# Kernel tuning notes

Hardware: AMD Instinct MI355X
Metric: run time of the kernel (lower is better)

## Reference

```python
import jax, jax.numpy as jnp
import numpy as np

N, E, HID, INP = 100000, 1600000, 64, 3
BN_EPS = 1e-5


def _bn(h, gamma, beta):
    # BatchNorm1d in training mode: biased batch stats over dim 0
    m = jnp.mean(h, axis=0)
    v = jnp.mean((h - m) ** 2, axis=0)
    return (h - m) * jax.lax.rsqrt(v + BN_EPS) * gamma + beta


def setup_inputs() -> dict:
    key = jax.random.key(0)
    ks = jax.random.split(key, 16)
    d_in = INP + HID  # 67
    s1 = 1.0 / np.sqrt(d_in)
    s2 = 1.0 / np.sqrt(HID)
    return {
        "x": jax.random.normal(ks[0], (N, INP), jnp.float32),
        "edge_index": jax.random.randint(ks[1], (2, E), 0, N, jnp.int64),
        "edge_attr": jax.random.normal(ks[2], (E, HID), jnp.float32),
        "u": jax.random.normal(ks[3], (1, 16), jnp.float32),
        "batch": jnp.zeros((N,), jnp.int64),
        # node_mlp_1: Linear(67,64), BN(64), ReLU, Linear(64,64)
        "w1": jax.random.uniform(ks[4], (d_in, HID), jnp.float32, -s1, s1),
        "b1": jax.random.uniform(ks[5], (HID,), jnp.float32, -s1, s1),
        "g1": jnp.ones((HID,), jnp.float32),
        "be1": jnp.zeros((HID,), jnp.float32),
        "w2": jax.random.uniform(ks[6], (HID, HID), jnp.float32, -s2, s2),
        "b2": jax.random.uniform(ks[7], (HID,), jnp.float32, -s2, s2),
        # node_mlp_2: Linear(67,64), BN(64), ReLU, Linear(64,64)
        "w3": jax.random.uniform(ks[8], (d_in, HID), jnp.float32, -s1, s1),
        "b3": jax.random.uniform(ks[9], (HID,), jnp.float32, -s1, s1),
        "g3": jnp.ones((HID,), jnp.float32),
        "be3": jnp.zeros((HID,), jnp.float32),
        "w4": jax.random.uniform(ks[10], (HID, HID), jnp.float32, -s2, s2),
        "b4": jax.random.uniform(ks[11], (HID,), jnp.float32, -s2, s2),
    }


def reference(x, edge_index, edge_attr, u, batch,
              w1, b1, g1, be1, w2, b2,
              w3, b3, g3, be3, w4, b4):
    row, col = edge_index[0], edge_index[1]
    n = x.shape[0]
    # gather source nodes, concat with edge features -> edge MLP
    h = jnp.concatenate([x[row], edge_attr], axis=1)          # [E, 67]
    h = _bn(h @ w1 + b1, g1, be1)
    h = jax.nn.relu(h) @ w2 + b2                              # [E, 64]
    # scatter_mean by destination node (0 for isolated nodes)
    s = jax.ops.segment_sum(h, col, num_segments=n)           # [N, 64]
    cnt = jax.ops.segment_sum(jnp.ones((h.shape[0],), h.dtype), col, num_segments=n)
    agg = s / jnp.maximum(cnt, 1.0)[:, None]
    # node MLP
    o = jnp.concatenate([x, agg], axis=1)                     # [N, 67]
    o = _bn(o @ w3 + b3, g3, be3)
    return jax.nn.relu(o) @ w4 + b4                           # [N, 64]
```

## Files before the change

### kernel.cpp

```cpp
#include <hip/hip_runtime.h>


#define HID 64
#define KPAD 104
#define RPAD 72
#define BN_EPS 1e-5f

typedef __attribute__((ext_vector_type(8))) short bf16x8;
typedef __attribute__((ext_vector_type(4))) short bf16x4;
typedef __attribute__((ext_vector_type(4))) float f32x4;

static __device__ __forceinline__ short f2bf(float f) {
  union { float fv; unsigned u; } v; v.fv = f;
  unsigned r = v.u + 0x7FFFu + ((v.u >> 16) & 1u);
  return (short)(r >> 16);
}

static __device__ __forceinline__ void stage_w_k96(short (*W)[KPAD], const float* __restrict__ w, int tid) {
  for (int i = tid; i < 64 * KPAD; i += 256) {
    int n = i / KPAD, k = i - n * KPAD;
    float v = 0.f;
    if (k < 64)      v = w[(size_t)(3 + k) * HID + n];
    else if (k < 67) v = w[(size_t)(k - 64) * HID + n];
    W[n][k] = f2bf(v);
  }
}

static __device__ __forceinline__ void stage_w_k64(short (*W)[RPAD], const float* __restrict__ w, int tid) {
  for (int i = tid; i < 64 * RPAD; i += 256) {
    int n = i / RPAD, k = i - n * RPAD;
    float v = (k < 64) ? w[(size_t)k * HID + n] : 0.f;
    W[n][k] = f2bf(v);
  }
}

static __device__ __forceinline__ void gemm_k96(const short (*A)[KPAD], const short (*W)[KPAD],
                                                int wv, int l15, int kg, f32x4* acc) {
  const int ar = wv * 16 + l15;
  #pragma unroll
  for (int ks = 0; ks < 3; ++ks) {
    bf16x8 a = *(const bf16x8*)&A[ar][ks * 32 + kg * 8];
    #pragma unroll
    for (int j = 0; j < 4; ++j) {
      bf16x8 b = *(const bf16x8*)&W[j * 16 + l15][ks * 32 + kg * 8];
      acc[j] = __builtin_amdgcn_mfma_f32_16x16x32_bf16(a, b, acc[j], 0, 0, 0);
    }
  }
}

static __device__ __forceinline__ void gemm_k64(const short (*A)[RPAD], const short (*W)[RPAD],
                                                int wv, int l15, int kg, f32x4* acc) {
  const int ar = wv * 16 + l15;
  #pragma unroll
  for (int ks = 0; ks < 2; ++ks) {
    bf16x8 a = *(const bf16x8*)&A[ar][ks * 32 + kg * 8];
    #pragma unroll
    for (int j = 0; j < 4; ++j) {
      bf16x8 b = *(const bf16x8*)&W[j * 16 + l15][ks * 32 + kg * 8];
      acc[j] = __builtin_amdgcn_mfma_f32_16x16x32_bf16(a, b, acc[j], 0, 0, 0);
    }
  }
}

static __device__ __forceinline__ void stage_edge_A(short (*A)[KPAD], const float* __restrict__ attr,
                                                    const int* __restrict__ ei_row,
                                                    const float* __restrict__ x,
                                                    long e0, int E, int tid) {
  #pragma unroll
  for (int u = 0; u < 4; ++u) {
    int f4 = tid + u * 256;
    int r = f4 >> 4, c4 = (f4 & 15) << 2;
    long e = e0 + r;
    float4 v = make_float4(0.f, 0.f, 0.f, 0.f);
    if (e < E) v = *reinterpret_cast<const float4*>(attr + (size_t)e * HID + c4);
    bf16x4 s; s[0] = f2bf(v.x); s[1] = f2bf(v.y); s[2] = f2bf(v.z); s[3] = f2bf(v.w);
    *reinterpret_cast<bf16x4*>(&A[r][c4]) = s;
  }
  if (tid < 64) {
    long e = e0 + tid;
    float x0 = 0.f, x1 = 0.f, x2 = 0.f;
    if (e < E) {
      int nd = ei_row[e];
      x0 = x[nd * 3]; x1 = x[nd * 3 + 1]; x2 = x[nd * 3 + 2];
    }
    A[tid][64] = f2bf(x0); A[tid][65] = f2bf(x1); A[tid][66] = f2bf(x2);
  }
}

static __device__ __forceinline__ void stage_node_A(short (*A)[KPAD], const float* __restrict__ aggsum,
                                                    const float* __restrict__ cnt,
                                                    const float* __restrict__ x,
                                                    long n0, int N, int tid) {
  #pragma unroll
  for (int u = 0; u < 4; ++u) {
    int f4 = tid + u * 256;
    int r = f4 >> 4, c4 = (f4 & 15) << 2;
    long n = n0 + r;
    float4 v = make_float4(0.f, 0.f, 0.f, 0.f);
    if (n < N) {
      float ic = 1.f / fmaxf(cnt[n], 1.f);
      const float4 t = *reinterpret_cast<const float4*>(aggsum + (size_t)n * HID + c4);
      v.x = t.x * ic; v.y = t.y * ic; v.z = t.z * ic; v.w = t.w * ic;
    }
    bf16x4 s; s[0] = f2bf(v.x); s[1] = f2bf(v.y); s[2] = f2bf(v.z); s[3] = f2bf(v.w);
    *reinterpret_cast<bf16x4*>(&A[r][c4]) = s;
  }
  if (tid < 64) {
    long n = n0 + tid;
    float x0 = 0.f, x1 = 0.f, x2 = 0.f;
    if (n < N) { x0 = x[n * 3]; x1 = x[n * 3 + 1]; x2 = x[n * 3 + 2]; }
    A[tid][64] = f2bf(x0); A[tid][65] = f2bf(x1); A[tid][66] = f2bf(x2);
  }
}

__global__ __launch_bounds__(256) void k_edge_stats(
    const float* __restrict__ attr, const int* __restrict__ ei_row,
    const float* __restrict__ x, const float* __restrict__ w1,
    float* __restrict__ gsum, float* __restrict__ gsq, int E, int numTiles) {
  __shared__ short A[64][KPAD];
  __shared__ short W1s[64][KPAD];
  __shared__ float redS[64], redQ[64];

  const int tid = threadIdx.x;
  const int lane = tid & 63, wv = tid >> 6;
  const int l15 = lane & 15, kg = lane >> 4;

  for (int i = tid; i < 64 * KPAD; i += 256) ((short*)A)[i] = 0;
  stage_w_k96(W1s, w1, tid);
  if (tid < 64) { redS[tid] = 0.f; redQ[tid] = 0.f; }

  float rs[4] = {0.f, 0.f, 0.f, 0.f};
  float rq[4] = {0.f, 0.f, 0.f, 0.f};

  for (int tile = blockIdx.x; tile < numTiles; tile += gridDim.x) {
    __syncthreads();
    stage_edge_A(A, attr, ei_row, x, (long)tile * 64, E, tid);
    __syncthreads();
    f32x4 acc[4];
    const f32x4 z = {0.f, 0.f, 0.f, 0.f};
    acc[0] = z; acc[1] = z; acc[2] = z; acc[3] = z;
    gemm_k96(A, W1s, wv, l15, kg, acc);
    #pragma unroll
    for (int j = 0; j < 4; ++j) {
      float s = 0.f, q = 0.f;
      #pragma unroll
      for (int rg = 0; rg < 4; ++rg) { float v = acc[j][rg]; s += v; q += v * v; }
      rs[j] += s; rq[j] += q;
    }
  }
  __syncthreads();
  #pragma unroll
  for (int j = 0; j < 4; ++j) {
    atomicAdd(&redS[j * 16 + l15], rs[j]);
    atomicAdd(&redQ[j * 16 + l15], rq[j]);
  }
  __syncthreads();
  if (tid < 64) { atomicAdd(&gsum[tid], redS[tid]); atomicAdd(&gsq[tid], redQ[tid]); }
}

__global__ void k_finalize(const float* __restrict__ gsum, const float* __restrict__ gsq,
                           const float* __restrict__ g, const float* __restrict__ be,
                           float* __restrict__ scale, float* __restrict__ shift, float denom) {
  int t = threadIdx.x;
  if (t < 64) {
    float m = gsum[t] / denom;
    float var = gsq[t] / denom - m * m;
    float is = rsqrtf(var + BN_EPS);
    float sc = g[t] * is;
    scale[t] = sc;
    shift[t] = be[t] - m * sc;
  }
}

__global__ __launch_bounds__(256) void k_edge_main(
    const float* __restrict__ attr, const int* __restrict__ ei_row,
    const int* __restrict__ ei_col, const float* __restrict__ x,
    const float* __restrict__ w1, const float* __restrict__ w2,
    const float* __restrict__ b2, const float* __restrict__ scaleE,
    const float* __restrict__ shiftE,
    float* __restrict__ aggsum, float* __restrict__ cnt, int E, int numTiles) {
  __shared__ short A[64][KPAD];
  __shared__ short W1s[64][KPAD];
  __shared__ short R[64][RPAD];
  __shared__ short W2s[64][RPAD];
  __shared__ float sclS[64], shtS[64], b2S[64];
  __shared__ int colS[64];

  const int tid = threadIdx.x;
  const int lane = tid & 63, wv = tid >> 6;
  const int l15 = lane & 15, kg = lane >> 4;

  for (int i = tid; i < 64 * KPAD; i += 256) ((short*)A)[i] = 0;
  stage_w_k96(W1s, w1, tid);
  stage_w_k64(W2s, w2, tid);
  if (tid < 64) { sclS[tid] = scaleE[tid]; shtS[tid] = shiftE[tid]; b2S[tid] = b2[tid]; }

  const f32x4 z = {0.f, 0.f, 0.f, 0.f};

  for (int tile = blockIdx.x; tile < numTiles; tile += gridDim.x) {
    __syncthreads();
    stage_edge_A(A, attr, ei_row, x, (long)tile * 64, E, tid);
    if (tid < 64) {
      long e = (long)tile * 64 + tid;
      int c = (e < E) ? ei_col[e] : -1;
      colS[tid] = c;
      if (c >= 0) atomicAdd(&cnt[c], 1.f);
    }
    __syncthreads();

    f32x4 acc1[4];
    acc1[0] = z; acc1[1] = z; acc1[2] = z; acc1[3] = z;
    gemm_k96(A, W1s, wv, l15, kg, acc1);

    #pragma unroll
    for (int j = 0; j < 4; ++j) {
      int c = j * 16 + l15;
      float sc = sclS[c], sh = shtS[c];
      #pragma unroll
      for (int rg = 0; rg < 4; ++rg) {
        float v = fmaxf(acc1[j][rg] * sc + sh, 0.f);
        R[wv * 16 + kg * 4 + rg][c] = f2bf(v);
      }
    }
    __syncthreads();

    f32x4 acc2[4];
    acc2[0] = z; acc2[1] = z; acc2[2] = z; acc2[3] = z;
    gemm_k64(R, W2s, wv, l15, kg, acc2);

    #pragma unroll
    for (int j = 0; j < 4; ++j) {
      int c = j * 16 + l15;
      float bb = b2S[c];
      #pragma unroll
      for (int rg = 0; rg < 4; ++rg) {
        int nd = colS[wv * 16 + kg * 4 + rg];
        if (nd >= 0) atomicAdd(&aggsum[(size_t)nd * HID + c], acc2[j][rg] + bb);
      }
    }
  }
}

__global__ __launch_bounds__(256) void k_node_stats(
    const float* __restrict__ aggsum, const float* __restrict__ cnt,
    const float* __restrict__ x, const float* __restrict__ w3,
    float* __restrict__ gsum, float* __restrict__ gsq, int N, int numTiles) {
  __shared__ short A[64][KPAD];
  __shared__ short W3s[64][KPAD];
  __shared__ float redS[64], redQ[64];

  const int tid = threadIdx.x;
  const int lane = tid & 63, wv = tid >> 6;
  const int l15 = lane & 15, kg = lane >> 4;

  for (int i = tid; i < 64 * KPAD; i += 256) ((short*)A)[i] = 0;
  stage_w_k96(W3s, w3, tid);
  if (tid < 64) { redS[tid] = 0.f; redQ[tid] = 0.f; }

  float rs[4] = {0.f, 0.f, 0.f, 0.f};
  float rq[4] = {0.f, 0.f, 0.f, 0.f};

  for (int tile = blockIdx.x; tile < numTiles; tile += gridDim.x) {
    __syncthreads();
    stage_node_A(A, aggsum, cnt, x, (long)tile * 64, N, tid);
    __syncthreads();
    f32x4 acc[4];
    const f32x4 z = {0.f, 0.f, 0.f, 0.f};
    acc[0] = z; acc[1] = z; acc[2] = z; acc[3] = z;
    gemm_k96(A, W3s, wv, l15, kg, acc);
    #pragma unroll
    for (int j = 0; j < 4; ++j) {
      float s = 0.f, q = 0.f;
      #pragma unroll
      for (int rg = 0; rg < 4; ++rg) { float v = acc[j][rg]; s += v; q += v * v; }
      rs[j] += s; rq[j] += q;
    }
  }
  __syncthreads();
  #pragma unroll
  for (int j = 0; j < 4; ++j) {
    atomicAdd(&redS[j * 16 + l15], rs[j]);
    atomicAdd(&redQ[j * 16 + l15], rq[j]);
  }
  __syncthreads();
  if (tid < 64) { atomicAdd(&gsum[tid], redS[tid]); atomicAdd(&gsq[tid], redQ[tid]); }
}

__global__ __launch_bounds__(256) void k_node_main(
    const float* __restrict__ aggsum, const float* __restrict__ cnt,
    const float* __restrict__ x, const float* __restrict__ w3,
    const float* __restrict__ w4, const float* __restrict__ b4,
    const float* __restrict__ scaleN, const float* __restrict__ shiftN,
    float* __restrict__ out, int N, int numTiles) {
  __shared__ short A[64][KPAD];
  __shared__ short W3s[64][KPAD];
  __shared__ short R[64][RPAD];
  __shared__ short W4s[64][RPAD];
  __shared__ float sclS[64], shtS[64], b4S[64];

  const int tid = threadIdx.x;
  const int lane = tid & 63, wv = tid >> 6;
  const int l15 = lane & 15, kg = lane >> 4;

  for (int i = tid; i < 64 * KPAD; i += 256) ((short*)A)[i] = 0;
  stage_w_k96(W3s, w3, tid);
  stage_w_k64(W4s, w4, tid);
  if (tid < 64) { sclS[tid] = scaleN[tid]; shtS[tid] = shiftN[tid]; b4S[tid] = b4[tid]; }

  const f32x4 z = {0.f, 0.f, 0.f, 0.f};

  for (int tile = blockIdx.x; tile < numTiles; tile += gridDim.x) {
    __syncthreads();
    stage_node_A(A, aggsum, cnt, x, (long)tile * 64, N, tid);
    __syncthreads();

    f32x4 acc1[4];
    acc1[0] = z; acc1[1] = z; acc1[2] = z; acc1[3] = z;
    gemm_k96(A, W3s, wv, l15, kg, acc1);

    #pragma unroll
    for (int j = 0; j < 4; ++j) {
      int c = j * 16 + l15;
      float sc = sclS[c], sh = shtS[c];
      #pragma unroll
      for (int rg = 0; rg < 4; ++rg) {
        float v = fmaxf(acc1[j][rg] * sc + sh, 0.f);
        R[wv * 16 + kg * 4 + rg][c] = f2bf(v);
      }
    }
    __syncthreads();

    f32x4 acc2[4];
    acc2[0] = z; acc2[1] = z; acc2[2] = z; acc2[3] = z;
    gemm_k64(R, W4s, wv, l15, kg, acc2);

    long n0 = (long)tile * 64;
    #pragma unroll
    for (int j = 0; j < 4; ++j) {
      int c = j * 16 + l15;
      float bb = b4S[c];
      #pragma unroll
      for (int rg = 0; rg < 4; ++rg) {
        long n = n0 + wv * 16 + kg * 4 + rg;
        if (n < N) out[(size_t)n * HID + c] = acc2[j][rg] + bb;
      }
    }
  }
}

extern "C" void kernel_launch(void* const* d_in, const int* in_sizes, int n_in,
                              void* d_out, int out_size, void* d_ws, size_t ws_size,
                              hipStream_t stream) {
  const float* x    = (const float*)d_in[0];
  const int*   ei   = (const int*)d_in[1];
  const float* attr = (const float*)d_in[2];
  const float* w1   = (const float*)d_in[5];
  const float* g1   = (const float*)d_in[7];
  const float* be1  = (const float*)d_in[8];
  const float* w2   = (const float*)d_in[9];
  const float* b2   = (const float*)d_in[10];
  const float* w3   = (const float*)d_in[11];
  const float* g3   = (const float*)d_in[13];
  const float* be3  = (const float*)d_in[14];
  const float* w4   = (const float*)d_in[15];
  const float* b4   = (const float*)d_in[16];
  float* out = (float*)d_out;

  const int N = in_sizes[0] / 3;
  const int E = in_sizes[1] / 2;

  float* wsf = (float*)d_ws;
  float* gsumE  = wsf + 0;
  float* gsqE   = wsf + 64;
  float* scaleE = wsf + 128;
  float* shiftE = wsf + 192;
  float* gsumN  = wsf + 256;
  float* gsqN   = wsf + 320;
  float* scaleN = wsf + 384;
  float* shiftN = wsf + 448;
  float* aggsum = wsf + 512;
  float* cnt    = wsf + 512 + (size_t)N * HID;

  hipMemsetAsync(d_ws, 0, (512 + (size_t)N * HID + (size_t)N) * sizeof(float), stream);

  const int tilesE = (E + 63) / 64;
  const int tilesN = (N + 63) / 64;
  const int gridE = tilesE < 2048 ? tilesE : 2048;

  k_edge_stats<<<gridE, 256, 0, stream>>>(attr, ei, x, w1, gsumE, gsqE, E, tilesE);
  k_finalize<<<1, 64, 0, stream>>>(gsumE, gsqE, g1, be1, scaleE, shiftE, (float)E);
  k_edge_main<<<gridE, 256, 0, stream>>>(attr, ei, ei + E, x, w1, w2, b2, scaleE, shiftE,
                                         aggsum, cnt, E, tilesE);
  k_node_stats<<<tilesN, 256, 0, stream>>>(aggsum, cnt, x, w3, gsumN, gsqN, N, tilesN);
  k_finalize<<<1, 64, 0, stream>>>(gsumN, gsqN, g3, be3, scaleN, shiftN, (float)N);
  k_node_main<<<tilesN, 256, 0, stream>>>(aggsum, cnt, x, w3, w4, b4, scaleN, shiftN, out, N, tilesN);
}
```

Baseline: 1.211 ms.

## Scatter ReLU activations before second linear, fp16 atomics, register-resident weights

Uses the linearity of the second edge Linear to scatter-add the post-ReLU activations per destination node and apply W2 and b2 once per node in a new kernel. This removes the per-edge second GEMM and cuts atomic traffic. Scatter atomics now use packed half2 in an fp16 accumulator, halving scatter bytes. Weights are held as MFMA B fragments in registers with wave-level 16-row tiles instead of shared-memory staging and block barriers, and node activations are stored as bf16. The fp16 accumulation risks precision loss and overflow on high-degree nodes.

```diff
diff --git a/kernel.cpp b/kernel.cpp
--- a/kernel.cpp
+++ b/kernel.cpp
@@ -1,8 +1,8 @@
 #include <hip/hip_runtime.h>
+#include <hip/hip_fp16.h>
 
 
 #define HID 64
-#define KPAD 104
 #define RPAD 72
 #define BN_EPS 1e-5f
 
@@ -16,130 +16,113 @@
   return (short)(r >> 16);
 }
 
-static __device__ __forceinline__ void stage_w_k96(short (*W)[KPAD], const float* __restrict__ w, int tid) {
-  for (int i = tid; i < 64 * KPAD; i += 256) {
-    int n = i / KPAD, k = i - n * KPAD;
-    float v = 0.f;
-    if (k < 64)      v = w[(size_t)(3 + k) * HID + n];
-    else if (k < 67) v = w[(size_t)(k - 64) * HID + n];
-    W[n][k] = f2bf(v);
-  }
-}
-
-static __device__ __forceinline__ void stage_w_k64(short (*W)[RPAD], const float* __restrict__ w, int tid) {
-  for (int i = tid; i < 64 * RPAD; i += 256) {
-    int n = i / RPAD, k = i - n * RPAD;
-    float v = (k < 64) ? w[(size_t)k * HID + n] : 0.f;
-    W[n][k] = f2bf(v);
-  }
-}
-
-static __device__ __forceinline__ void gemm_k96(const short (*A)[KPAD], const short (*W)[KPAD],
-                                                int wv, int l15, int kg, f32x4* acc) {
-  const int ar = wv * 16 + l15;
+#define Z8 {0,0,0,0,0,0,0,0}
+
+static __device__ __forceinline__ void load_B96(bf16x8 Bf[3][4], const float* __restrict__ w,
+                                                int l15, int kg) {
   #pragma unroll
-  for (int ks = 0; ks < 3; ++ks) {
-    bf16x8 a = *(const bf16x8*)&A[ar][ks * 32 + kg * 8];
-    #pragma unroll
-    for (int j = 0; j < 4; ++j) {
-      bf16x8 b = *(const bf16x8*)&W[j * 16 + l15][ks * 32 + kg * 8];
-      acc[j] = __builtin_amdgcn_mfma_f32_16x16x32_bf16(a, b, acc[j], 0, 0, 0);
-    }
-  }
-}
-
-static __device__ __forceinline__ void gemm_k64(const short (*A)[RPAD], const short (*W)[RPAD],
-                                                int wv, int l15, int kg, f32x4* acc) {
-  const int ar = wv * 16 + l15;
+  for (int ks = 0; ks < 3; ++ks)
+    #pragma unroll
+    for (int j = 0; j < 4; ++j) {
+      bf16x8 b = Z8;
+      #pragma unroll
+      for (int jj = 0; jj < 8; ++jj) {
+        int k = ks * 32 + kg * 8 + jj;
+        int n = 4 * l15 + j;
+        float v = 0.f;
+        if (k < 64)      v = w[(size_t)(3 + k) * HID + n];
+        else if (k < 67) v = w[(size_t)(k - 64) * HID + n];
+        b[jj] = f2bf(v);
+      }
+      Bf[ks][j] = b;
+    }
+}
+
+static __device__ __forceinline__ void load_B64(bf16x8 Bf[2][4], const float* __restrict__ w,
+                                                int l15, int kg) {
   #pragma unroll
-  for (int ks = 0; ks < 2; ++ks) {
-    bf16x8 a = *(const bf16x8*)&A[ar][ks * 32 + kg * 8];
-    #pragma unroll
-    for (int j = 0; j < 4; ++j) {
-      bf16x8 b = *(const bf16x8*)&W[j * 16 + l15][ks * 32 + kg * 8];
-      acc[j] = __builtin_amdgcn_mfma_f32_16x16x32_bf16(a, b, acc[j], 0, 0, 0);
-    }
-  }
-}
-
-static __device__ __forceinline__ void stage_edge_A(short (*A)[KPAD], const float* __restrict__ attr,
-                                                    const int* __restrict__ ei_row,
-                                                    const float* __restrict__ x,
-                                                    long e0, int E, int tid) {
-  #pragma unroll
-  for (int u = 0; u < 4; ++u) {
-    int f4 = tid + u * 256;
-    int r = f4 >> 4, c4 = (f4 & 15) << 2;
-    long e = e0 + r;
-    float4 v = make_float4(0.f, 0.f, 0.f, 0.f);
-    if (e < E) v = *reinterpret_cast<const float4*>(attr + (size_t)e * HID + c4);
-    bf16x4 s; s[0] = f2bf(v.x); s[1] = f2bf(v.y); s[2] = f2bf(v.z); s[3] = f2bf(v.w);
-    *reinterpret_cast<bf16x4*>(&A[r][c4]) = s;
-  }
-  if (tid < 64) {
-    long e = e0 + tid;
-    float x0 = 0.f, x1 = 0.f, x2 = 0.f;
-    if (e < E) {
+  for (int ks = 0; ks < 2; ++ks)
+    #pragma unroll
+    for (int j = 0; j < 4; ++j) {
+      bf16x8 b = Z8;
+      #pragma unroll
+      for (int jj = 0; jj < 8; ++jj) {
+        int k = ks * 32 + kg * 8 + jj;
+        int n = 4 * l15 + j;
+        b[jj] = f2bf(w[(size_t)k * HID + n]);
+      }
+      Bf[ks][j] = b;
+    }
+}
+
+static __device__ __forceinline__ void edge_A(bf16x8 A[3], const float* __restrict__ attr,
+                                              const int* __restrict__ ei_row,
+                                              const float* __restrict__ x,
+                                              long e0, int E, int l15, int kg) {
+  bf16x8 a0 = Z8, a1 = Z8, a2 = Z8;
+  long e = e0 + l15;
+  if (e < E) {
+    const float* ar = attr + (size_t)e * HID + kg * 8;
+    f32x4 p0 = *(const f32x4*)(ar);
+    f32x4 p1 = *(const f32x4*)(ar + 4);
+    f32x4 p2 = *(const f32x4*)(ar + 32);
+    f32x4 p3 = *(const f32x4*)(ar + 36);
+    #pragma unroll
+    for (int t = 0; t < 4; ++t) {
+      a0[t] = f2bf(p0[t]); a0[4 + t] = f2bf(p1[t]);
+      a1[t] = f2bf(p2[t]); a1[4 + t] = f2bf(p3[t]);
+    }
+    if (kg == 0) {
       int nd = ei_row[e];
-      x0 = x[nd * 3]; x1 = x[nd * 3 + 1]; x2 = x[nd * 3 + 2];
-    }
-    A[tid][64] = f2bf(x0); A[tid][65] = f2bf(x1); A[tid][66] = f2bf(x2);
-  }
-}
-
-static __device__ __forceinline__ void stage_node_A(short (*A)[KPAD], const float* __restrict__ aggsum,
-                                                    const float* __restrict__ cnt,
-                                                    const float* __restrict__ x,
-                                                    long n0, int N, int tid) {
-  #pragma unroll
-  for (int u = 0; u < 4; ++u) {
-    int f4 = tid + u * 256;
-    int r = f4 >> 4, c4 = (f4 & 15) << 2;
-    long n = n0 + r;
-    float4 v = make_float4(0.f, 0.f, 0.f, 0.f);
-    if (n < N) {
-      float ic = 1.f / fmaxf(cnt[n], 1.f);
-      const float4 t = *reinterpret_cast<const float4*>(aggsum + (size_t)n * HID + c4);
-      v.x = t.x * ic; v.y = t.y * ic; v.z = t.z * ic; v.w = t.w * ic;
-    }
-    bf16x4 s; s[0] = f2bf(v.x); s[1] = f2bf(v.y); s[2] = f2bf(v.z); s[3] = f2bf(v.w);
-    *reinterpret_cast<bf16x4*>(&A[r][c4]) = s;
-  }
-  if (tid < 64) {
-    long n = n0 + tid;
-    float x0 = 0.f, x1 = 0.f, x2 = 0.f;
-    if (n < N) { x0 = x[n * 3]; x1 = x[n * 3 + 1]; x2 = x[n * 3 + 2]; }
-    A[tid][64] = f2bf(x0); A[tid][65] = f2bf(x1); A[tid][66] = f2bf(x2);
-  }
+      a2[0] = f2bf(x[(size_t)nd * 3]);
+      a2[1] = f2bf(x[(size_t)nd * 3 + 1]);
+      a2[2] = f2bf(x[(size_t)nd * 3 + 2]);
+    }
+  }
+  A[0] = a0; A[1] = a1; A[2] = a2;
+}
+
+static __device__ __forceinline__ void node_A(bf16x8 A[3], const short* __restrict__ aggb,
+                                              const float* __restrict__ x,
+                                              long n0, int N, int l15, int kg) {
+  bf16x8 a0 = Z8, a1 = Z8, a2 = Z8;
+  long n = n0 + l15;
+  if (n < N) {
+    a0 = *(const bf16x8*)(aggb + (size_t)n * HID + kg * 8);
+    a1 = *(const bf16x8*)(aggb + (size_t)n * HID + 32 + kg * 8);
+    if (kg == 0) {
+      a2[0] = f2bf(x[(size_t)n * 3]);
+      a2[1] = f2bf(x[(size_t)n * 3 + 1]);
+      a2[2] = f2bf(x[(size_t)n * 3 + 2]);
+    }
+  }
+  A[0] = a0; A[1] = a1; A[2] = a2;
 }
 
 __global__ __launch_bounds__(256) void k_edge_stats(
     const float* __restrict__ attr, const int* __restrict__ ei_row,
     const float* __restrict__ x, const float* __restrict__ w1,
     float* __restrict__ gsum, float* __restrict__ gsq, int E, int numTiles) {
-  __shared__ short A[64][KPAD];
-  __shared__ short W1s[64][KPAD];
-  __shared__ float redS[64], redQ[64];
-
   const int tid = threadIdx.x;
-  const int lane = tid & 63, wv = tid >> 6;
+  const int wv = tid >> 6, lane = tid & 63;
   const int l15 = lane & 15, kg = lane >> 4;
-
-  for (int i = tid; i < 64 * KPAD; i += 256) ((short*)A)[i] = 0;
-  stage_w_k96(W1s, w1, tid);
-  if (tid < 64) { redS[tid] = 0.f; redQ[tid] = 0.f; }
+  bf16x8 B[3][4];
+  load_B96(B, w1, l15, kg);
 
   float rs[4] = {0.f, 0.f, 0.f, 0.f};
   float rq[4] = {0.f, 0.f, 0.f, 0.f};
-
-  for (int tile = blockIdx.x; tile < numTiles; tile += gridDim.x) {
-    __syncthreads();
-    stage_edge_A(A, attr, ei_row, x, (long)tile * 64, E, tid);
-    __syncthreads();
-    f32x4 acc[4];
-    const f32x4 z = {0.f, 0.f, 0.f, 0.f};
-    acc[0] = z; acc[1] = z; acc[2] = z; acc[3] = z;
-    gemm_k96(A, W1s, wv, l15, kg, acc);
+  const f32x4 z = {0.f, 0.f, 0.f, 0.f};
+  const int wstride = gridDim.x * 4;
+
+  for (int t = blockIdx.x * 4 + wv; t < numTiles; t += wstride) {
+    bf16x8 A[3];
+    edge_A(A, attr, ei_row, x, (long)t * 16, E, l15, kg);
+    f32x4 acc[4]; acc[0] = z; acc[1] = z; acc[2] = z; acc[3] = z;
+    #pragma unroll
+    for (int ks = 0; ks < 3; ++ks)
+      #pragma unroll
+      for (int j = 0; j < 4; ++j)
+        acc[j] = __builtin_amdgcn_mfma_f32_16x16x32_bf16(A[ks], B[ks][j], acc[j], 0, 0, 0);
     #pragma unroll
     for (int j = 0; j < 4; ++j) {
       float s = 0.f, q = 0.f;
@@ -148,14 +131,18 @@
       rs[j] += s; rq[j] += q;
     }
   }
-  __syncthreads();
   #pragma unroll
   for (int j = 0; j < 4; ++j) {
-    atomicAdd(&redS[j * 16 + l15], rs[j]);
-    atomicAdd(&redQ[j * 16 + l15], rq[j]);
-  }
-  __syncthreads();
-  if (tid < 64) { atomicAdd(&gsum[tid], redS[tid]); atomicAdd(&gsq[tid], redQ[tid]); }
+    rs[j] += __shfl_xor(rs[j], 16); rs[j] += __shfl_xor(rs[j], 32);
+    rq[j] += __shfl_xor(rq[j], 16); rq[j] += __shfl_xor(rq[j], 32);
+  }
+  if (lane < 16) {
+    #pragma unroll
+    for (int j = 0; j < 4; ++j) {
+      atomicAdd(&gsum[4 * lane + j], rs[j]);
+      atomicAdd(&gsq[4 * lane + j], rq[j]);
+    }
+  }
 }
 
 __global__ void k_finalize(const float* __restrict__ gsum, const float* __restrict__ gsq,
@@ -175,99 +162,144 @@
 __global__ __launch_bounds__(256) void k_edge_main(
     const float* __restrict__ attr, const int* __restrict__ ei_row,
     const int* __restrict__ ei_col, const float* __restrict__ x,
-    const float* __restrict__ w1, const float* __restrict__ w2,
-    const float* __restrict__ b2, const float* __restrict__ scaleE,
+    const float* __restrict__ w1, const float* __restrict__ scaleE,
     const float* __restrict__ shiftE,
-    float* __restrict__ aggsum, float* __restrict__ cnt, int E, int numTiles) {
-  __shared__ short A[64][KPAD];
-  __shared__ short W1s[64][KPAD];
-  __shared__ short R[64][RPAD];
-  __shared__ short W2s[64][RPAD];
-  __shared__ float sclS[64], shtS[64], b2S[64];
-  __shared__ int colS[64];
-
+    __half* __restrict__ rsum, float* __restrict__ cnt, int E, int numTiles) {
   const int tid = threadIdx.x;
-  const int lane = tid & 63, wv = tid >> 6;
+  const int wv = tid >> 6, lane = tid & 63;
   const int l15 = lane & 15, kg = lane >> 4;
-
-  for (int i = tid; i < 64 * KPAD; i += 256) ((short*)A)[i] = 0;
-  stage_w_k96(W1s, w1, tid);
-  stage_w_k64(W2s, w2, tid);
-  if (tid < 64) { sclS[tid] = scaleE[tid]; shtS[tid] = shiftE[tid]; b2S[tid] = b2[tid]; }
+  bf16x8 B[3][4];
+  load_B96(B, w1, l15, kg);
+  const f32x4 scv = *(const f32x4*)(scaleE + 4 * l15);
+  const f32x4 shv = *(const f32x4*)(shiftE + 4 * l15);
 
   const f32x4 z = {0.f, 0.f, 0.f, 0.f};
-
-  for (int tile = blockIdx.x; tile < numTiles; tile += gridDim.x) {
-    __syncthreads();
-    stage_edge_A(A, attr, ei_row, x, (long)tile * 64, E, tid);
-    if (tid < 64) {
-      long e = (long)tile * 64 + tid;
-      int c = (e < E) ? ei_col[e] : -1;
-      colS[tid] = c;
-      if (c >= 0) atomicAdd(&cnt[c], 1.f);
-    }
-    __syncthreads();
-
-    f32x4 acc1[4];
-    acc1[0] = z; acc1[1] = z; acc1[2] = z; acc1[3] = z;
-    gemm_k96(A, W1s, wv, l15, kg, acc1);
-
-    #pragma unroll
-    for (int j = 0; j < 4; ++j) {
-      int c = j * 16 + l15;
-      float sc = sclS[c], sh = shtS[c];
-      #pragma unroll
-      for (int rg = 0; rg < 4; ++rg) {
-        float v = fmaxf(acc1[j][rg] * sc + sh, 0.f);
-        R[wv * 16 + kg * 4 + rg][c] = f2bf(v);
+  const int wstride = gridDim.x * 4;
+
+  for (int t = blockIdx.x * 4 + wv; t < numTiles; t += wstride) {
+    long e0 = (long)t * 16;
+    bf16x8 A[3];
+    edge_A(A, attr, ei_row, x, e0, E, l15, kg);
+
+    int carr[4];
+    #pragma unroll
+    for (int rg = 0; rg < 4; ++rg) {
+      long e = e0 + kg * 4 + rg;
+      carr[rg] = (e < E) ? ei_col[e] : -1;
+    }
+
+    f32x4 acc[4]; acc[0] = z; acc[1] = z; acc[2] = z; acc[3] = z;
+    #pragma unroll
+    for (int ks = 0; ks < 3; ++ks)
+      #pragma unroll
+      for (int j = 0; j < 4; ++j)
+        acc[j] = __builtin_amdgcn_mfma_f32_16x16x32_bf16(A[ks], B[ks][j], acc[j], 0, 0, 0);
+
+    if (l15 == 0) {
+      #pragma unroll
+      for (int rg = 0; rg < 4; ++rg)
+        if (carr[rg] >= 0) atomicAdd(&cnt[carr[rg]], 1.f);
+    }
+
+    #pragma unroll
+    for (int rg = 0; rg < 4; ++rg) {
+      int nd = carr[rg];
+      if (nd < 0) continue;
+      float v0 = fmaxf(acc[0][rg] * scv[0] + shv[0], 0.f);
+      float v1 = fmaxf(acc[1][rg] * scv[1] + shv[1], 0.f);
+      float v2 = fmaxf(acc[2][rg] * scv[2] + shv[2], 0.f);
+      float v3 = fmaxf(acc[3][rg] * scv[3] + shv[3], 0.f);
+      __half2 h01 = __halves2half2(__float2half(v0), __float2half(v1));
+      __half2 h23 = __halves2half2(__float2half(v2), __float2half(v3));
+      __half2* dst = (__half2*)(rsum + (size_t)nd * HID + 4 * l15);
+      unsafeAtomicAdd(dst, h01);
+      unsafeAtomicAdd(dst + 1, h23);
+    }
+  }
+}
+
+static __device__ __forceinline__ void unpack_h8(bf16x8& a, const __half* __restrict__ p, float ic) {
+  union { int4 i4; __half2 h[4]; } u;
+  u.i4 = *(const int4*)p;
+  #pragma unroll
+  for (int t = 0; t < 4; ++t) {
+    float2 f = __half22float2(u.h[t]);
+    a[2 * t]     = f2bf(f.x * ic);
+    a[2 * t + 1] = f2bf(f.y * ic);
+  }
+}
+
+__global__ __launch_bounds__(256) void k_node_agg(
+    const __half* __restrict__ rsum, const float* __restrict__ cnt,
+    const float* __restrict__ w2, const float* __restrict__ b2,
+    short* __restrict__ aggb, int N, int numTiles) {
+  const int tid = threadIdx.x;
+  const int wv = tid >> 6, lane = tid & 63;
+  const int l15 = lane & 15, kg = lane >> 4;
+  bf16x8 B[2][4];
+  load_B64(B, w2, l15, kg);
+  const f32x4 b2v = *(const f32x4*)(b2 + 4 * l15);
+
+  const f32x4 z = {0.f, 0.f, 0.f, 0.f};
+  const int wstride = gridDim.x * 4;
+
+  for (int t = blockIdx.x * 4 + wv; t < numTiles; t += wstride) {
+    long n0 = (long)t * 16;
+    long n = n0 + l15;
+    bf16x8 a0 = Z8, a1 = Z8;
+    if (n < N) {
+      float ic = 1.f / fmaxf(cnt[n], 1.f);
+      const __half* rr = rsum + (size_t)n * HID;
+      unpack_h8(a0, rr + kg * 8, ic);
+      unpack_h8(a1, rr + 32 + kg * 8, ic);
+    }
+    f32x4 acc[4]; acc[0] = z; acc[1] = z; acc[2] = z; acc[3] = z;
+    #pragma unroll
+    for (int j = 0; j < 4; ++j) {
+      acc[j] = __builtin_amdgcn_mfma_f32_16x16x32_bf16(a0, B[0][j], acc[j], 0, 0, 0);
+      acc[j] = __builtin_amdgcn_mfma_f32_16x16x32_bf16(a1, B[1][j], acc[j], 0, 0, 0);
+    }
+    long no = n0 + kg * 4;
+    #pragma unroll
+    for (int rg = 0; rg < 4; ++rg) {
+      long nr = no + rg;
+      if (nr >= N) continue;
+      bool has = (cnt[nr] > 0.f);
+      bf16x4 o;
+      #pragma unroll
+      for (int j = 0; j < 4; ++j) {
+        float v = has ? (acc[j][rg] + b2v[j]) : 0.f;
+        o[j] = f2bf(v);
       }
-    }
-    __syncthreads();
-
-    f32x4 acc2[4];
-    acc2[0] = z; acc2[1] = z; acc2[2] = z; acc2[3] = z;
-    gemm_k64(R, W2s, wv, l15, kg, acc2);
-
-    #pragma unroll
-    for (int j = 0; j < 4; ++j) {
-      int c = j * 16 + l15;
-      float bb = b2S[c];
-      #pragma unroll
-      for (int rg = 0; rg < 4; ++rg) {
-        int nd = colS[wv * 16 + kg * 4 + rg];
-        if (nd >= 0) atomicAdd(&aggsum[(size_t)nd * HID + c], acc2[j][rg] + bb);
-      }
+      *(bf16x4*)(aggb + (size_t)nr * HID + 4 * l15) = o;
     }
   }
 }
 
 __global__ __launch_bounds__(256) void k_node_stats(
-    const float* __restrict__ aggsum, const float* __restrict__ cnt,
-    const float* __restrict__ x, const float* __restrict__ w3,
+    const short* __restrict__ aggb, const float* __restrict__ x,
+    const float* __restrict__ w3,
     float* __restrict__ gsum, float* __restrict__ gsq, int N, int numTiles) {
-  __shared__ short A[64][KPAD];
-  __shared__ short W3s[64][KPAD];
-  __shared__ float redS[64], redQ[64];
-
   const int tid = threadIdx.x;
-  const int lane = tid & 63, wv = tid >> 6;
+  const int wv = tid >> 6, lane = tid & 63;
   const int l15 = lane & 15, kg = lane >> 4;
-
-  for (int i = tid; i < 64 * KPAD; i += 256) ((short*)A)[i] = 0;
-  stage_w_k96(W3s, w3, tid);
-  if (tid < 64) { redS[tid] = 0.f; redQ[tid] = 0.f; }
+  bf16x8 B[3][4];
+  load_B96(B, w3, l15, kg);
 
   float rs[4] = {0.f, 0.f, 0.f, 0.f};
   float rq[4] = {0.f, 0.f, 0.f, 0.f};
-
-  for (int tile = blockIdx.x; tile < numTiles; tile += gridDim.x) {
-    __syncthreads();
-    stage_node_A(A, aggsum, cnt, x, (long)tile * 64, N, tid);
-    __syncthreads();
-    f32x4 acc[4];
-    const f32x4 z = {0.f, 0.f, 0.f, 0.f};
-    acc[0] = z; acc[1] = z; acc[2] = z; acc[3] = z;
-    gemm_k96(A, W3s, wv, l15, kg, acc);
+  const f32x4 z = {0.f, 0.f, 0.f, 0.f};
+  const int wstride = gridDim.x * 4;
+
+  for (int t = blockIdx.x * 4 + wv; t < numTiles; t += wstride) {
+    bf16x8 A[3];
+    node_A(A, aggb, x, (long)t * 16, N, l15, kg);
+    f32x4 acc[4]; acc[0] = z; acc[1] = z; acc[2] = z; acc[3] = z;
+    #pragma unroll
+    for (int ks = 0; ks < 3; ++ks)
+      #pragma unroll
+      for (int j = 0; j < 4; ++j)
+        acc[j] = __builtin_amdgcn_mfma_f32_16x16x32_bf16(A[ks], B[ks][j], acc[j], 0, 0, 0);
     #pragma unroll
     for (int j = 0; j < 4; ++j) {
       float s = 0.f, q = 0.f;
@@ -276,74 +308,81 @@
       rs[j] += s; rq[j] += q;
     }
   }
-  __syncthreads();
   #pragma unroll
   for (int j = 0; j < 4; ++j) {
-    atomicAdd(&redS[j * 16 + l15], rs[j]);
-    atomicAdd(&redQ[j * 16 + l15], rq[j]);
-  }
-  __syncthreads();
-  if (tid < 64) { atomicAdd(&gsum[tid], redS[tid]); atomicAdd(&gsq[tid], redQ[tid]); }
-}
-
-__global__ __launch_bounds__(256) void k_node_main(
-    const float* __restrict__ aggsum, const float* __restrict__ cnt,
-    const float* __restrict__ x, const float* __restrict__ w3,
-    const float* __restrict__ w4, const float* __restrict__ b4,
-    const float* __restrict__ scaleN, const float* __restrict__ shiftN,
-    float* __restrict__ out, int N, int numTiles) {
-  __shared__ short A[64][KPAD];
-  __shared__ short W3s[64][KPAD];
-  __shared__ short R[64][RPAD];
-  __shared__ short W4s[64][RPAD];
-  __shared__ float sclS[64], shtS[64], b4S[64];
-
-  const int tid = threadIdx.x;
-  const int lane = tid & 63, wv = tid >> 6;
+    rs[j] += __shfl_xor(rs[j], 16); rs[j] += __shfl_xor(rs[j], 32);
+    rq[j] += __shfl_xor(rq[j], 16); rq[j] += __shfl_xor(rq[j], 32);
+  }
+  if (lane < 16) {
+    #pragma unroll
+    for (int j = 0; j < 4; ++j) {
+      atomicAdd(&gsum[4 * lane + j], rs[j]);
+      atomicAdd(&gsq[4 * lane + j], rq[j]);
+    }
+  }
+}
+
+__global__ __launch_bounds__(64) void k_node_main(
+    const short* __restrict__ aggb, const float* __restrict__ x,
+    const float* __restrict__ w3, const float* __restrict__ w4,
+    const float* __restrict__ b4, const float* __restrict__ scaleN,
+    const float* __restrict__ shiftN, float* __restrict__ out, int N, int numTiles) {
+  __shared__ short R[16][RPAD];
+  const int lane = threadIdx.x & 63;
   const int l15 = lane & 15, kg = lane >> 4;
-
-  for (int i = tid; i < 64 * KPAD; i += 256) ((short*)A)[i] = 0;
-  stage_w_k96(W3s, w3, tid);
-  stage_w_k64(W4s, w4, tid);
-  if (tid < 64) { sclS[tid] = scaleN[tid]; shtS[tid] = shiftN[tid]; b4S[tid] = b4[tid]; }
+  bf16x8 B3[3][4];
+  load_B96(B3, w3, l15, kg);
+  bf16x8 B4[2][4];
+  load_B64(B4, w4, l15, kg);
+  const f32x4 scv = *(const f32x4*)(scaleN + 4 * l15);
+  const f32x4 shv = *(const f32x4*)(shiftN + 4 * l15);
+  const f32x4 b4v = *(const f32x4*)(b4 + 4 * l15);
 
   const f32x4 z = {0.f, 0.f, 0.f, 0.f};
 
-  for (int tile = blockIdx.x; tile < numTiles; tile += gridDim.x) {
+  for (int t = blockIdx.x; t < numTiles; t += gridDim.x) {
+    long n0 = (long)t * 16;
+    bf16x8 A[3];
+    node_A(A, aggb, x, n0, N, l15, kg);
+
+    f32x4 acc1[4]; acc1[0] = z; acc1[1] = z; acc1[2] = z; acc1[3] = z;
+    #pragma unroll
+    for (int ks = 0; ks < 3; ++ks)
+      #pragma unroll
+      for (int j = 0; j < 4; ++j)
+        acc1[j] = __builtin_amdgcn_mfma_f32_16x16x32_bf16(A[ks], B3[ks][j], acc1[j], 0, 0, 0);
+
     __syncthreads();
-    stage_node_A(A, aggsum, cnt, x, (long)tile * 64, N, tid);
+    #pragma unroll
+    for (int rg = 0; rg < 4; ++rg) {
+      bf16x4 o;
+      #pragma unroll
+      for (int j = 0; j < 4; ++j) {
+        float v = fmaxf(acc1[j][rg] * scv[j] + shv[j], 0.f);
+        o[j] = f2bf(v);
+      }
+      *(bf16x4*)&R[kg * 4 + rg][4 * l15] = o;
+    }
     __syncthreads();
 
-    f32x4 acc1[4];
-    acc1[0] = z; acc1[1] = z; acc1[2] = z; acc1[3] = z;
-    gemm_k96(A, W3s, wv, l15, kg, acc1);
-
-    #pragma unroll
-    for (int j = 0; j < 4; ++j) {
-      int c = j * 16 + l15;
-      float sc = sclS[c], sh = shtS[c];
-      #pragma unroll
-      for (int rg = 0; rg < 4; ++rg) {
-        float v = fmaxf(acc1[j][rg] * sc + sh, 0.f);
-        R[wv * 16 + kg * 4 + rg][c] = f2bf(v);
-      }
-    }
-    __syncthreads();
-
-    f32x4 acc2[4];
-    acc2[0] = z; acc2[1] = z; acc2[2] = z; acc2[3] = z;
-    gemm_k64(R, W4s, wv, l15, kg, acc2);
-
-    long n0 = (long)tile * 64;
-    #pragma unroll
-    for (int j = 0; j < 4; ++j) {
-      int c = j * 16 + l15;
-      float bb = b4S[c];
-      #pragma unroll
-      for (int rg = 0; rg < 4; ++rg) {
-        long n = n0 + wv * 16 + kg * 4 + rg;
-        if (n < N) out[(size_t)n * HID + c] = acc2[j][rg] + bb;
-      }
+    f32x4 acc2[4]; acc2[0] = z; acc2[1] = z; acc2[2] = z; acc2[3] = z;
+    #pragma unroll
+    for (int ks = 0; ks < 2; ++ks) {
+      bf16x8 a = *(const bf16x8*)&R[l15][ks * 32 + kg * 8];
+      #pragma unroll
+      for (int j = 0; j < 4; ++j)
+        acc2[j] = __builtin_amdgcn_mfma_f32_16x16x32_bf16(a, B4[ks][j], acc2[j], 0, 0, 0);
+    }
+
+    long no = n0 + kg * 4;
+    #pragma unroll
+    for (int rg = 0; rg < 4; ++rg) {
+      long nr = no + rg;
+      if (nr >= N) continue;
+      f32x4 o;
+      #pragma unroll
+      for (int j = 0; j < 4; ++j) o[j] = acc2[j][rg] + b4v[j];
+      *(f32x4*)(out + (size_t)nr * HID + 4 * l15) = o;
     }
   }
 }
@@ -378,20 +417,24 @@
   float* gsqN   = wsf + 320;
   float* scaleN = wsf + 384;
   float* shiftN = wsf + 448;
-  float* aggsum = wsf + 512;
-  float* cnt    = wsf + 512 + (size_t)N * HID;
-
-  hipMemsetAsync(d_ws, 0, (512 + (size_t)N * HID + (size_t)N) * sizeof(float), stream);
-
-  const int tilesE = (E + 63) / 64;
-  const int tilesN = (N + 63) / 64;
-  const int gridE = tilesE < 2048 ? tilesE : 2048;
+  __half* rsum  = (__half*)(wsf + 512);
+  float*  cnt   = wsf + 512 + (size_t)N * 32;
+  short*  aggb  = (short*)(wsf + 512 + (size_t)N * 33);
+
+  hipMemsetAsync(d_ws, 0, (512 + (size_t)N * 33) * sizeof(float), stream);
+
+  const int tilesE = (E + 15) / 16;
+  const int tilesN = (N + 15) / 16;
+  const int gridE = 2048;
+  const int gridN = 1024;
+  const int gridM = tilesN < 4096 ? tilesN : 4096;
 
   k_edge_stats<<<gridE, 256, 0, stream>>>(attr, ei, x, w1, gsumE, gsqE, E, tilesE);
   k_finalize<<<1, 64, 0, stream>>>(gsumE, gsqE, g1, be1, scaleE, shiftE, (float)E);
-  k_edge_main<<<gridE, 256, 0, stream>>>(attr, ei, ei + E, x, w1, w2, b2, scaleE, shiftE,
-                                         aggsum, cnt, E, tilesE);
-  k_node_stats<<<tilesN, 256, 0, stream>>>(aggsum, cnt, x, w3, gsumN, gsqN, N, tilesN);
+  k_edge_main<<<gridE, 256, 0, stream>>>(attr, ei, ei + E, x, w1, scaleE, shiftE,
+                                         rsum, cnt, E, tilesE);
+  k_node_agg<<<gridN, 256, 0, stream>>>(rsum, cnt, w2, b2, aggb, N, tilesN);
+  k_node_stats<<<gridN, 256, 0, stream>>>(aggb, x, w3, gsumN, gsqN, N, tilesN);
   k_finalize<<<1, 64, 0, stream>>>(gsumN, gsqN, g3, be3, scaleN, shiftN, (float)N);
-  k_node_main<<<tilesN, 256, 0, stream>>>(aggsum, cnt, x, w3, w4, b4, scaleN, shiftN, out, N, tilesN);
-}
+  k_node_main<<<gridM, 64, 0, stream>>>(aggb, x, w3, w4, b4, scaleN, shiftN, out, N, tilesN);
+}
```

New measurement: 2.129 ms. 1.76x slower.
